# Kernel optimization log

Measured on AMD Instinct MI355X. Metric: run time of the kernel, lower is better.

## Reference

```python
import jax, jax.numpy as jnp
import numpy as np

B, T, NX = 4, 6, 128
F_IN, H, F_OUT = 64, 128, 64
N = T * NX * NX  # 98304 cubed-sphere nodes


def _build_neighbors():
    # 4-neighbor grid adjacency per tile (periodic within tile), [N, 4] int32.
    t = np.arange(T)[:, None, None]
    i = np.arange(NX)[None, :, None]
    j = np.arange(NX)[None, None, :]

    def nid(tt, ii, jj):
        return tt * NX * NX + (ii % NX) * NX + (jj % NX)

    nbr = np.stack(
        [nid(t, i - 1, j), nid(t, i + 1, j), nid(t, i, j - 1), nid(t, i, j + 1)],
        axis=-1,
    ).reshape(-1, 4)
    return jnp.asarray(nbr, dtype=jnp.int32)


def setup_inputs() -> dict:
    key = jax.random.key(0)
    ks = jax.random.split(key, 20)
    inp = {
        "inputs": jax.random.normal(ks[0], (B, T, NX, NX, F_IN), dtype=jnp.float32),
        "nbr": _build_neighbors(),
    }
    # SAGEConv channel chain: 64->128, 128->64, 64->32, 32->32, 64->64, 128->64
    dims = [(F_IN, H), (H, H // 2), (H // 2, H // 4), (H // 4, H // 4), (H // 2, H // 2), (H, F_OUT)]
    k = 1
    for li, (din, dout) in enumerate(dims, start=1):
        s = 1.0 / np.sqrt(din)
        inp[f"W_self_{li}"] = jax.random.normal(ks[k], (din, dout), dtype=jnp.float32) * s
        inp[f"W_neigh_{li}"] = jax.random.normal(ks[k + 1], (din, dout), dtype=jnp.float32) * s
        inp[f"b_{li}"] = jnp.zeros((dout,), dtype=jnp.float32)
        k += 2
    return inp


def _sage(h, nbr, Ws, Wn, b):
    # h: [N, B, F]. Mean over the 4 fixed grid neighbors, then self+neighbor linear.
    m = (h[nbr[:, 0]] + h[nbr[:, 1]] + h[nbr[:, 2]] + h[nbr[:, 3]]) * 0.25
    return h @ Ws + m @ Wn + b


def reference(inputs, nbr,
              W_self_1, W_neigh_1, b_1, W_self_2, W_neigh_2, b_2,
              W_self_3, W_neigh_3, b_3, W_self_4, W_neigh_4, b_4,
              W_self_5, W_neigh_5, b_5, W_self_6, W_neigh_6, b_6):
    b, t, nx, ny, f = inputs.shape
    x = inputs.reshape(b, t * nx * ny, f).transpose(1, 0, 2)  # [N, B, F]
    act = jax.nn.relu
    # num_blocks = 1
    h1 = act(_sage(x, nbr, W_self_1, W_neigh_1, b_1))
    h2 = act(_sage(h1, nbr, W_self_2, W_neigh_2, b_2))
    h3 = act(_sage(h2, nbr, W_self_3, W_neigh_3, b_3))
    h4 = act(_sage(h3, nbr, W_self_4, W_neigh_4, b_4))
    h5 = jnp.concatenate([act(_sage(h4, nbr, W_self_4, W_neigh_4, b_4)), h3], axis=-1)
    h6 = jnp.concatenate([act(_sage(h5, nbr, W_self_5, W_neigh_5, b_5)), h2], axis=-1)
    out = _sage(h6, nbr, W_self_6, W_neigh_6, b_6)  # [N, B, F_OUT]
    return out.transpose(1, 0, 2).reshape(b, t, nx, ny, -1)
```

## Files before the change

kernel.cpp:

```cpp
#include <hip/hip_runtime.h>
#include <type_traits>

#define NNODES 98304
#define NB 4

typedef __attribute__((ext_vector_type(8))) short short8;
typedef __attribute__((ext_vector_type(8))) unsigned short ushort8;
typedef __attribute__((ext_vector_type(4))) float f32x4;

__device__ __forceinline__ float bf2f(unsigned short u) {
  union { unsigned int u; float f; } c; c.u = ((unsigned int)u) << 16; return c.f;
}
__device__ __forceinline__ unsigned short f2bf(float f) {
  union { float f; unsigned int u; } c; c.f = f;
  unsigned int r = 0x7FFFu + ((c.u >> 16) & 1u);
  return (unsigned short)((c.u + r) >> 16);
}
__device__ __forceinline__ unsigned int cvtpk(float lo, float hi) {
  unsigned int r;
  asm("v_cvt_pk_bf16_f32 %0, %1, %2" : "=v"(r) : "v"(lo), "v"(hi));
  return r;
}

__device__ __forceinline__ void tile_barrier() {
  asm volatile("s_waitcnt lgkmcnt(0)" ::: "memory");
  __builtin_amdgcn_s_barrier();
  asm volatile("" ::: "memory");
}

constexpr int rows_for(int FIN)            { return FIN == 32 ? 64 : 32; }
constexpr int grid_for(int FIN, int SRCK)  { return (FIN == 128 || SRCK == 0) ? 1024 : 1536; }
constexpr int minw_for(int FIN, int SRCK)  { return (FIN == 128 || SRCK == 0) ? 4 : 6; }

template<int FIN, int FOUT, int SRCK, int DSTK, bool RELU>
__global__ __launch_bounds__(256, minw_for(FIN, SRCK))
void sage_mfma(const void* __restrict__ srcp, int sstride, int soff,
               void* __restrict__ dstp, int dstride, int doff,
               const float* __restrict__ Ws, const float* __restrict__ Wn,
               const float* __restrict__ bias, const int* __restrict__ nbr)
{
  constexpr int ROWS = rows_for(FIN);
  constexpr int GRID = grid_for(FIN, SRCK);
  constexpr int NPT = ROWS / 4;
  constexpr int NTILES = (NNODES * NB) / ROWS;
  constexpr int K = 2 * FIN;
  constexpr int KSTEPS = K / 32;
  constexpr int LD = K + 8;
  constexpr int WAVES_N = (FOUT >= 64) ? 4 : 2;
  constexpr int WAVES_M = 4 / WAVES_N;
  constexpr int CF = FOUT / (16 * WAVES_N);
  constexpr int RF = ROWS / (16 * WAVES_M);
  constexpr int CHUNKS = FIN / 8;
  constexpr int ITERS = (ROWS * CHUNKS) / 256;
  constexpr int PF = ITERS;
  constexpr int PT = ITERS - PF;

  __shared__ unsigned short As[2][ROWS][LD];

  const int tid = threadIdx.x;
  const int wave = tid >> 6, lane = tid & 63;
  const int wn = wave % WAVES_N, wm = wave / WAVES_N;
  const int colbase = wn * (FOUT / WAVES_N);
  const int rowbase = wm * (ROWS / WAVES_M);
  const int fn = lane & 15, fg = lane >> 4;

  short8 Bfrag[KSTEPS][CF];
  float bv[CF];
  #pragma unroll
  for (int ks = 0; ks < KSTEPS; ++ks) {
    const float* wb = (ks * 32 < FIN) ? (Ws + (size_t)(ks * 32) * FOUT)
                                      : (Wn + (size_t)(ks * 32 - FIN) * FOUT);
    #pragma unroll
    for (int cf = 0; cf < CF; ++cf) {
      const int col = colbase + cf * 16 + fn;
      short8 f;
      #pragma unroll
      for (int j = 0; j < 8; ++j)
        f[j] = (short)f2bf(wb[(size_t)(fg * 8 + j) * FOUT + col]);
      Bfrag[ks][cf] = f;
    }
  }
  #pragma unroll
  for (int cf = 0; cf < CF; ++cf) bv[cf] = bias[colbase + cf * 16 + fn];

  struct G0 { float4 s0, s1, a0, a1, b0, b1, c0, c1, d0, d1; };
  struct G1 { ushort8 s, n0, n1, n2, n3; };
  using PG = typename std::conditional<SRCK == 0, G0, G1>::type;

  auto issue = [&](int node0, int it, PG& p) {
    const int g = tid + it * 256;
    const int r = g / CHUNKS;
    const int c = (g - r * CHUNKS) * 8;
    const int n = node0 + (r >> 2);
    const int b = r & 3;
    const int4 nb4 = reinterpret_cast<const int4*>(nbr)[n];
    if constexpr (SRCK == 0) {
      const float* s = (const float*)srcp;
      const float* ps = s + ((size_t)b * NNODES + n) * FIN + c;
      const float* p0 = s + ((size_t)b * NNODES + nb4.x) * FIN + c;
      const float* p1 = s + ((size_t)b * NNODES + nb4.y) * FIN + c;
      const float* p2 = s + ((size_t)b * NNODES + nb4.z) * FIN + c;
      const float* p3 = s + ((size_t)b * NNODES + nb4.w) * FIN + c;
      p.s0 = *(const float4*)ps; p.s1 = *(const float4*)(ps + 4);
      p.a0 = *(const float4*)p0; p.a1 = *(const float4*)(p0 + 4);
      p.b0 = *(const float4*)p1; p.b1 = *(const float4*)(p1 + 4);
      p.c0 = *(const float4*)p2; p.c1 = *(const float4*)(p2 + 4);
      p.d0 = *(const float4*)p3; p.d1 = *(const float4*)(p3 + 4);
    } else {
      const unsigned short* s = (const unsigned short*)srcp;
      auto ld = [&](int nn) {
        return *reinterpret_cast<const ushort8*>(s + ((size_t)nn * NB + b) * sstride + soff + c);
      };
      p.s = ld(n); p.n0 = ld(nb4.x); p.n1 = ld(nb4.y); p.n2 = ld(nb4.z); p.n3 = ld(nb4.w);
    }
  };

  auto finish = [&](int buf, int it, PG& p) {
    const int g = tid + it * 256;
    const int r = g / CHUNKS;
    const int c = (g - r * CHUNKS) * 8;
    uint4 xv, mv;
    if constexpr (SRCK == 0) {
      xv = make_uint4(cvtpk(p.s0.x, p.s0.y), cvtpk(p.s0.z, p.s0.w),
                      cvtpk(p.s1.x, p.s1.y), cvtpk(p.s1.z, p.s1.w));
      float4 m0, m1;
      m0.x = (p.a0.x + p.b0.x) + (p.c0.x + p.d0.x);
      m0.y = (p.a0.y + p.b0.y) + (p.c0.y + p.d0.y);
      m0.z = (p.a0.z + p.b0.z) + (p.c0.z + p.d0.z);
      m0.w = (p.a0.w + p.b0.w) + (p.c0.w + p.d0.w);
      m1.x = (p.a1.x + p.b1.x) + (p.c1.x + p.d1.x);
      m1.y = (p.a1.y + p.b1.y) + (p.c1.y + p.d1.y);
      m1.z = (p.a1.z + p.b1.z) + (p.c1.z + p.d1.z);
      m1.w = (p.a1.w + p.b1.w) + (p.c1.w + p.d1.w);
      mv = make_uint4(cvtpk(m0.x * 0.25f, m0.y * 0.25f), cvtpk(m0.z * 0.25f, m0.w * 0.25f),
                      cvtpk(m1.x * 0.25f, m1.y * 0.25f), cvtpk(m1.z * 0.25f, m1.w * 0.25f));
    } else {
      xv = make_uint4((unsigned)(unsigned short)p.s[0] | ((unsigned)(unsigned short)p.s[1] << 16),
                      (unsigned)(unsigned short)p.s[2] | ((unsigned)(unsigned short)p.s[3] << 16),
                      (unsigned)(unsigned short)p.s[4] | ((unsigned)(unsigned short)p.s[5] << 16),
                      (unsigned)(unsigned short)p.s[6] | ((unsigned)(unsigned short)p.s[7] << 16));
      float sum[8];
      #pragma unroll
      for (int j = 0; j < 8; ++j)
        sum[j] = (bf2f(p.n0[j]) + bf2f(p.n1[j])) + (bf2f(p.n2[j]) + bf2f(p.n3[j]));
      mv = make_uint4(cvtpk(sum[0] * 0.25f, sum[1] * 0.25f), cvtpk(sum[2] * 0.25f, sum[3] * 0.25f),
                      cvtpk(sum[4] * 0.25f, sum[5] * 0.25f), cvtpk(sum[6] * 0.25f, sum[7] * 0.25f));
    }
    *reinterpret_cast<uint4*>(&As[buf][r][c]) = xv;
    *reinterpret_cast<uint4*>(&As[buf][r][FIN + c]) = mv;
  };

  {
    PG p[ITERS];
    #pragma unroll
    for (int it = 0; it < ITERS; ++it) issue(blockIdx.x * NPT, it, p[it]);
    #pragma unroll
    for (int it = 0; it < ITERS; ++it) finish(0, it, p[it]);
  }

  int cur = 0;
  for (int tile = blockIdx.x; tile < NTILES; tile += GRID) {
    const int node0 = tile * NPT;
    const bool hasnext = (tile + GRID) < NTILES;
    const int nnode0 = (tile + GRID) * NPT;

    PG ptop[PF];
    if (hasnext) {
      #pragma unroll
      for (int it = 0; it < PF; ++it) issue(nnode0, it, ptop[it]);
    }

    tile_barrier();

    f32x4 acc[RF][CF];
    #pragma unroll
    for (int rf = 0; rf < RF; ++rf)
      #pragma unroll
      for (int cf = 0; cf < CF; ++cf)
        acc[rf][cf] = (f32x4){bv[cf], bv[cf], bv[cf], bv[cf]};

    #pragma unroll
    for (int ks = 0; ks < KSTEPS; ++ks) {
      short8 a[RF];
      #pragma unroll
      for (int rf = 0; rf < RF; ++rf)
        a[rf] = *reinterpret_cast<const short8*>(&As[cur][rowbase + rf * 16 + fn][ks * 32 + fg * 8]);
      #pragma unroll
      for (int rf = 0; rf < RF; ++rf)
        #pragma unroll
        for (int cf = 0; cf < CF; ++cf)
          acc[rf][cf] = __builtin_amdgcn_mfma_f32_16x16x32_bf16(
              a[rf], Bfrag[ks][cf], acc[rf][cf], 0, 0, 0);
    }

    #pragma unroll
    for (int rf = 0; rf < RF; ++rf) {
      #pragma unroll
      for (int cf = 0; cf < CF; ++cf) {
        const int col = colbase + cf * 16 + fn;
        #pragma unroll
        for (int j = 0; j < 4; ++j) {
          const int row = rowbase + rf * 16 + fg * 4 + j;
          const int n = node0 + (row >> 2);
          const int b = row & 3;
          float v = acc[rf][cf][j];
          if (RELU) v = fmaxf(v, 0.f);
          if (DSTK == 0) {
            ((float*)dstp)[((size_t)b * NNODES + n) * FOUT + col] = v;
          } else {
            ((unsigned short*)dstp)[((size_t)n * NB + b) * dstride + doff + col] = f2bf(v);
          }
        }
      }
    }

    if (hasnext) {
      #pragma unroll
      for (int it = 0; it < PF; ++it) finish(cur ^ 1, it, ptop[it]);
    }
    cur ^= 1;
  }
}

extern "C" void kernel_launch(void* const* d_in, const int* in_sizes, int n_in,
                              void* d_out, int out_size, void* d_ws, size_t ws_size,
                              hipStream_t stream) {
  const float* x  = (const float*)d_in[0];
  const int* nbr  = (const int*)d_in[1];
  const float* W1s = (const float*)d_in[2],  *W1n = (const float*)d_in[3],  *b1 = (const float*)d_in[4];
  const float* W2s = (const float*)d_in[5],  *W2n = (const float*)d_in[6],  *b2 = (const float*)d_in[7];
  const float* W3s = (const float*)d_in[8],  *W3n = (const float*)d_in[9],  *b3 = (const float*)d_in[10];
  const float* W4s = (const float*)d_in[11], *W4n = (const float*)d_in[12], *b4 = (const float*)d_in[13];
  const float* W5s = (const float*)d_in[14], *W5n = (const float*)d_in[15], *b5 = (const float*)d_in[16];
  const float* W6s = (const float*)d_in[17], *W6n = (const float*)d_in[18], *b6 = (const float*)d_in[19];

  unsigned short* h1 = (unsigned short*)d_out;
  unsigned short* h6 = (unsigned short*)d_ws;
  unsigned short* h5 = (unsigned short*)d_out;
  unsigned short* h4 = (unsigned short*)((char*)d_out + (size_t)NNODES * NB * 64 * 2);

  const dim3 block(256);

  sage_mfma<64, 128, 0, 1, true><<<dim3(grid_for(64, 0)), block, 0, stream>>>(x, 0, 0, h1, 128, 0, W1s, W1n, b1, nbr);
  sage_mfma<128, 64, 1, 1, true><<<dim3(grid_for(128, 1)), block, 0, stream>>>(h1, 128, 0, h6, 128, 64, W2s, W2n, b2, nbr);
  sage_mfma<64, 32, 1, 1, true><<<dim3(grid_for(64, 1)), block, 0, stream>>>(h6, 128, 64, h5, 64, 32, W3s, W3n, b3, nbr);
  sage_mfma<32, 32, 1, 1, true><<<dim3(grid_for(32, 1)), block, 0, stream>>>(h5, 64, 32, h4, 32, 0, W4s, W4n, b4, nbr);
  sage_mfma<32, 32, 1, 1, true><<<dim3(grid_for(32, 1)), block, 0, stream>>>(h4, 32, 0, h5, 64, 0, W4s, W4n, b4, nbr);
  sage_mfma<64, 64, 1, 1, true><<<dim3(grid_for(64, 1)), block, 0, stream>>>(h5, 64, 0, h6, 128, 0, W5s, W5n, b5, nbr);
  sage_mfma<128, 64, 1, 0, false><<<dim3(grid_for(128, 1)), block, 0, stream>>>(h6, 128, 0, d_out, 0, 0, W6s, W6n, b6, nbr);
}
```

Before: 229.3 us.

## Fuse pairs of SAGE layers with halo-tiled stencil kernels on grid tiles

Replaces the generic neighbor-index gather with spatial 8x8 tiles plus halos loaded into LDS, exploiting the periodic grid stencil directly. Pairs of consecutive layers (1-2, 4-4, 5-6) are fused so the intermediate activation stays in LDS and is recomputed on a halo ring instead of going through global memory. Weights are pre-transposed to bf16 in a device global buffer by small prep kernels. This trades redundant halo recomputation, larger LDS use and extra prep launches for fewer global round trips and fewer kernel launches. It also ignores the nbr input and assumes the fixed grid adjacency.

```diff
diff --git a/kernel.cpp b/kernel.cpp
--- a/kernel.cpp
+++ b/kernel.cpp
@@ -3,6 +3,8 @@
 
 #define NNODES 98304
 #define NB 4
+#define NX 128
+#define FACE (NX * NX)
 
 typedef __attribute__((ext_vector_type(8))) short short8;
 typedef __attribute__((ext_vector_type(8))) unsigned short ushort8;
@@ -10,6 +12,9 @@
 
 __device__ __forceinline__ float bf2f(unsigned short u) {
   union { unsigned int u; float f; } c; c.u = ((unsigned int)u) << 16; return c.f;
+}
+__device__ __forceinline__ float asf(unsigned int u) {
+  union { unsigned int u; float f; } c; c.u = u; return c.f;
 }
 __device__ __forceinline__ unsigned short f2bf(float f) {
   union { float f; unsigned int u; } c; c.f = f;
@@ -22,12 +27,204 @@
   return r;
 }
 
+__device__ __forceinline__ short8 mean4(const unsigned short* pA, const unsigned short* pB,
+                                        const unsigned short* pC, const unsigned short* pD) {
+  uint4 a = *(const uint4*)pA, b = *(const uint4*)pB, c = *(const uint4*)pC, d = *(const uint4*)pD;
+  const unsigned* pa = &a.x; const unsigned* pb = &b.x;
+  const unsigned* pc = &c.x; const unsigned* pd = &d.x;
+  union { uint4 u; short8 s; } o;
+  unsigned* po = &o.u.x;
+  #pragma unroll
+  for (int i = 0; i < 4; ++i) {
+    float lo = (asf(pa[i] << 16) + asf(pb[i] << 16)) + (asf(pc[i] << 16) + asf(pd[i] << 16));
+    float hi = (asf(pa[i] & 0xFFFF0000u) + asf(pb[i] & 0xFFFF0000u)) +
+               (asf(pc[i] & 0xFFFF0000u) + asf(pd[i] & 0xFFFF0000u));
+    po[i] = cvtpk(lo * 0.25f, hi * 0.25f);
+  }
+  return o.s;
+}
+
+__device__ __attribute__((aligned(16))) unsigned short g_wt[59392];
+#define WT_A12 0
+#define WT_B12 16384
+#define WT_45  32768
+#define WT_A67 34816
+#define WT_B67 43008
+
+__global__ void prep_wt(const float* __restrict__ Ws, const float* __restrict__ Wn,
+                        int FIN, int FOUT, int dstoff) {
+  const int K = 2 * FIN, total = FOUT * K;
+  for (int e = blockIdx.x * 256 + threadIdx.x; e < total; e += gridDim.x * 256) {
+    const int col = e / K, k = e % K;
+    const float v = (k < FIN) ? Ws[(size_t)k * FOUT + col] : Wn[(size_t)(k - FIN) * FOUT + col];
+    g_wt[dstoff + e] = f2bf(v);
+  }
+}
+
+template<int FA, int FOA, int FEXT, int FOB, int SRCK, int DSTK, bool RELUB, int MINW>
+__global__ __launch_bounds__(256, MINW)
+void sage_fused2(const void* __restrict__ srcA, int ssA, int soA,
+                 const unsigned short* __restrict__ srcE, int ssE, int soE,
+                 void* __restrict__ dst, int dstr, int dof,
+                 int wtaOff, int wtbOff,
+                 const float* __restrict__ ba, const float* __restrict__ bb)
+{
+  constexpr int TI = 8, TJ = 8;
+  constexpr int RAJ = TJ + 4, NRA = (TI + 4) * RAJ;
+  constexpr int HJ = TJ + 2, NH = (TI + 2) * HJ;
+  constexpr int MA = 112;
+  constexpr int KA = 2 * FA, KB = 2 * (FOA + FEXT);
+  constexpr int CFA = FOA / 16, CFB = FOB / 16;
+  constexpr int LDA = FA + 8, LDH = FOA + 8, LDE = FEXT + 8;
+
+  __shared__ unsigned short rawA[NRA][LDA];
+  __shared__ unsigned short H[MA][LDH];
+  __shared__ unsigned short rawE[FEXT ? NH : 1][FEXT ? LDE : 1];
+
+  const int tid = threadIdx.x;
+  const int b = blockIdx.x & 3;
+  const int tt = blockIdx.x >> 2;
+  const int t = tt >> 8;
+  const int i0 = ((tt >> 4) & 15) * TI, j0 = (tt & 15) * TJ;
+  const int nbase = t * FACE;
+
+  constexpr int CHA = FA / 8;
+  for (int u = tid; u < NRA * CHA; u += 256) {
+    const int s = u / CHA, c = (u - s * CHA) * 8;
+    const int di = s / RAJ - 2, dj = s % RAJ - 2;
+    const int n = nbase + ((i0 + di) & (NX - 1)) * NX + ((j0 + dj) & (NX - 1));
+    uint4 v;
+    if constexpr (SRCK == 0) {
+      const float* p = (const float*)srcA + ((size_t)b * NNODES + n) * FA + c;
+      const float4 a = *(const float4*)p, q = *(const float4*)(p + 4);
+      v = make_uint4(cvtpk(a.x, a.y), cvtpk(a.z, a.w), cvtpk(q.x, q.y), cvtpk(q.z, q.w));
+    } else {
+      v = *(const uint4*)((const unsigned short*)srcA + ((size_t)n * NB + b) * ssA + soA + c);
+    }
+    *(uint4*)&rawA[s][c] = v;
+  }
+  if constexpr (FEXT != 0) {
+    constexpr int CHE = FEXT / 8;
+    for (int u = tid; u < NH * CHE; u += 256) {
+      const int s = u / CHE, c = (u - s * CHE) * 8;
+      const int di = s / HJ - 1, dj = s % HJ - 1;
+      const int n = nbase + ((i0 + di) & (NX - 1)) * NX + ((j0 + dj) & (NX - 1));
+      *(uint4*)&rawE[s][c] =
+          *(const uint4*)(srcE + ((size_t)n * NB + b) * ssE + soE + c);
+    }
+  }
+  __syncthreads();
+
+  const int lane = tid & 63, wave = tid >> 6;
+  const int fn = lane & 15, fg = lane >> 4;
+
+  {
+    const unsigned short* wt = g_wt + wtaOff;
+    #pragma unroll 1
+    for (int rfi = 0; rfi < 2; ++rfi) {
+      const int rf = wave + rfi * 4;
+      if (rf >= 7) break;
+      const int r = rf * 16 + fn;
+      const int rc = r < NH ? r : NH - 1;
+      const int sA = (rc / HJ + 1) * RAJ + (rc % HJ) + 1;
+      f32x4 acc[CFA];
+      #pragma unroll
+      for (int cf = 0; cf < CFA; ++cf) {
+        const float4 bt = *(const float4*)(ba + cf * 16 + fg * 4);
+        acc[cf] = (f32x4){bt.x, bt.y, bt.z, bt.w};
+      }
+      #pragma unroll 1
+      for (int ks = 0; ks < KA / 32; ++ks) {
+        short8 xf;
+        if (ks < FA / 32) {
+          xf = *(const short8*)&rawA[sA][ks * 32 + fg * 8];
+        } else {
+          const int cc = (ks - FA / 32) * 32 + fg * 8;
+          xf = mean4(&rawA[sA - RAJ][cc], &rawA[sA + RAJ][cc],
+                     &rawA[sA - 1][cc], &rawA[sA + 1][cc]);
+        }
+        #pragma unroll
+        for (int cf = 0; cf < CFA; ++cf) {
+          const short8 wf = *(const short8*)(wt + (size_t)(cf * 16 + fn) * KA + ks * 32 + fg * 8);
+          acc[cf] = __builtin_amdgcn_mfma_f32_16x16x32_bf16(wf, xf, acc[cf], 0, 0, 0);
+        }
+      }
+      #pragma unroll
+      for (int cf = 0; cf < CFA; ++cf) {
+        const uint2 u = make_uint2(
+            cvtpk(fmaxf(acc[cf][0], 0.f), fmaxf(acc[cf][1], 0.f)),
+            cvtpk(fmaxf(acc[cf][2], 0.f), fmaxf(acc[cf][3], 0.f)));
+        *(uint2*)&H[r][cf * 16 + fg * 4] = u;
+      }
+    }
+  }
+  __syncthreads();
+
+  {
+    const unsigned short* wt = g_wt + wtbOff;
+    const int r = wave * 16 + fn;
+    const int sH = (r / TJ + 1) * HJ + (r % TJ) + 1;
+    f32x4 acc[CFB];
+    #pragma unroll
+    for (int cf = 0; cf < CFB; ++cf) {
+      const float bt = bb[cf * 16 + fn];
+      acc[cf] = (f32x4){bt, bt, bt, bt};
+    }
+    constexpr int S1 = FOA / 32;
+    constexpr int S2 = S1 + FEXT / 32;
+    constexpr int S3 = S2 + FOA / 32;
+    #pragma unroll 1
+    for (int ks = 0; ks < KB / 32; ++ks) {
+      short8 xf;
+      if constexpr (FEXT == 0) {
+        if (ks < S1) {
+          xf = *(const short8*)&H[sH][ks * 32 + fg * 8];
+        } else {
+          const int cc = (ks - S1) * 32 + fg * 8;
+          xf = mean4(&H[sH - HJ][cc], &H[sH + HJ][cc], &H[sH - 1][cc], &H[sH + 1][cc]);
+        }
+      } else {
+        if (ks < S1) {
+          xf = *(const short8*)&H[sH][ks * 32 + fg * 8];
+        } else if (ks < S2) {
+          xf = *(const short8*)&rawE[sH][(ks - S1) * 32 + fg * 8];
+        } else if (ks < S3) {
+          const int cc = (ks - S2) * 32 + fg * 8;
+          xf = mean4(&H[sH - HJ][cc], &H[sH + HJ][cc], &H[sH - 1][cc], &H[sH + 1][cc]);
+        } else {
+          const int cc = (ks - S3) * 32 + fg * 8;
+          xf = mean4(&rawE[sH - HJ][cc], &rawE[sH + HJ][cc], &rawE[sH - 1][cc], &rawE[sH + 1][cc]);
+        }
+      }
+      #pragma unroll
+      for (int cf = 0; cf < CFB; ++cf) {
+        const short8 wf = *(const short8*)(wt + (size_t)(cf * 16 + fn) * KB + ks * 32 + fg * 8);
+        acc[cf] = __builtin_amdgcn_mfma_f32_16x16x32_bf16(xf, wf, acc[cf], 0, 0, 0);
+      }
+    }
+    #pragma unroll
+    for (int cf = 0; cf < CFB; ++cf) {
+      const int col = cf * 16 + fn;
+      #pragma unroll
+      for (int j = 0; j < 4; ++j) {
+        const int rr = wave * 16 + fg * 4 + j;
+        const int n = nbase + (i0 + (rr / TJ)) * NX + j0 + (rr % TJ);
+        float v = acc[cf][j];
+        if (RELUB) v = fmaxf(v, 0.f);
+        if constexpr (DSTK == 0)
+          ((float*)dst)[((size_t)b * NNODES + n) * FOB + col] = v;
+        else
+          ((unsigned short*)dst)[((size_t)n * NB + b) * dstr + dof + col] = f2bf(v);
+      }
+    }
+  }
+}
+
 __device__ __forceinline__ void tile_barrier() {
   asm volatile("s_waitcnt lgkmcnt(0)" ::: "memory");
   __builtin_amdgcn_s_barrier();
   asm volatile("" ::: "memory");
 }
-
 constexpr int rows_for(int FIN)            { return FIN == 32 ? 64 : 32; }
 constexpr int grid_for(int FIN, int SRCK)  { return (FIN == 128 || SRCK == 0) ? 1024 : 1536; }
 constexpr int minw_for(int FIN, int SRCK)  { return (FIN == 128 || SRCK == 0) ? 4 : 6; }
@@ -53,7 +250,6 @@
   constexpr int CHUNKS = FIN / 8;
   constexpr int ITERS = (ROWS * CHUNKS) / 256;
   constexpr int PF = ITERS;
-  constexpr int PT = ITERS - PF;
 
   __shared__ unsigned short As[2][ROWS][LD];
 
@@ -83,9 +279,8 @@
   #pragma unroll
   for (int cf = 0; cf < CF; ++cf) bv[cf] = bias[colbase + cf * 16 + fn];
 
-  struct G0 { float4 s0, s1, a0, a1, b0, b1, c0, c1, d0, d1; };
   struct G1 { ushort8 s, n0, n1, n2, n3; };
-  using PG = typename std::conditional<SRCK == 0, G0, G1>::type;
+  using PG = G1;
 
   auto issue = [&](int node0, int it, PG& p) {
     const int g = tid + it * 256;
@@ -94,58 +289,27 @@
     const int n = node0 + (r >> 2);
     const int b = r & 3;
     const int4 nb4 = reinterpret_cast<const int4*>(nbr)[n];
-    if constexpr (SRCK == 0) {
-      const float* s = (const float*)srcp;
-      const float* ps = s + ((size_t)b * NNODES + n) * FIN + c;
-      const float* p0 = s + ((size_t)b * NNODES + nb4.x) * FIN + c;
-      const float* p1 = s + ((size_t)b * NNODES + nb4.y) * FIN + c;
-      const float* p2 = s + ((size_t)b * NNODES + nb4.z) * FIN + c;
-      const float* p3 = s + ((size_t)b * NNODES + nb4.w) * FIN + c;
-      p.s0 = *(const float4*)ps; p.s1 = *(const float4*)(ps + 4);
-      p.a0 = *(const float4*)p0; p.a1 = *(const float4*)(p0 + 4);
-      p.b0 = *(const float4*)p1; p.b1 = *(const float4*)(p1 + 4);
-      p.c0 = *(const float4*)p2; p.c1 = *(const float4*)(p2 + 4);
-      p.d0 = *(const float4*)p3; p.d1 = *(const float4*)(p3 + 4);
-    } else {
-      const unsigned short* s = (const unsigned short*)srcp;
-      auto ld = [&](int nn) {
-        return *reinterpret_cast<const ushort8*>(s + ((size_t)nn * NB + b) * sstride + soff + c);
-      };
-      p.s = ld(n); p.n0 = ld(nb4.x); p.n1 = ld(nb4.y); p.n2 = ld(nb4.z); p.n3 = ld(nb4.w);
-    }
+    const unsigned short* s = (const unsigned short*)srcp;
+    auto ld = [&](int nn) {
+      return *reinterpret_cast<const ushort8*>(s + ((size_t)nn * NB + b) * sstride + soff + c);
+    };
+    p.s = ld(n); p.n0 = ld(nb4.x); p.n1 = ld(nb4.y); p.n2 = ld(nb4.z); p.n3 = ld(nb4.w);
   };
-
   auto finish = [&](int buf, int it, PG& p) {
     const int g = tid + it * 256;
     const int r = g / CHUNKS;
     const int c = (g - r * CHUNKS) * 8;
-    uint4 xv, mv;
-    if constexpr (SRCK == 0) {
-      xv = make_uint4(cvtpk(p.s0.x, p.s0.y), cvtpk(p.s0.z, p.s0.w),
-                      cvtpk(p.s1.x, p.s1.y), cvtpk(p.s1.z, p.s1.w));
-      float4 m0, m1;
-      m0.x = (p.a0.x + p.b0.x) + (p.c0.x + p.d0.x);
-      m0.y = (p.a0.y + p.b0.y) + (p.c0.y + p.d0.y);
-      m0.z = (p.a0.z + p.b0.z) + (p.c0.z + p.d0.z);
-      m0.w = (p.a0.w + p.b0.w) + (p.c0.w + p.d0.w);
-      m1.x = (p.a1.x + p.b1.x) + (p.c1.x + p.d1.x);
-      m1.y = (p.a1.y + p.b1.y) + (p.c1.y + p.d1.y);
-      m1.z = (p.a1.z + p.b1.z) + (p.c1.z + p.d1.z);
-      m1.w = (p.a1.w + p.b1.w) + (p.c1.w + p.d1.w);
-      mv = make_uint4(cvtpk(m0.x * 0.25f, m0.y * 0.25f), cvtpk(m0.z * 0.25f, m0.w * 0.25f),
-                      cvtpk(m1.x * 0.25f, m1.y * 0.25f), cvtpk(m1.z * 0.25f, m1.w * 0.25f));
-    } else {
-      xv = make_uint4((unsigned)(unsigned short)p.s[0] | ((unsigned)(unsigned short)p.s[1] << 16),
-                      (unsigned)(unsigned short)p.s[2] | ((unsigned)(unsigned short)p.s[3] << 16),
-                      (unsigned)(unsigned short)p.s[4] | ((unsigned)(unsigned short)p.s[5] << 16),
-                      (unsigned)(unsigned short)p.s[6] | ((unsigned)(unsigned short)p.s[7] << 16));
-      float sum[8];
-      #pragma unroll
-      for (int j = 0; j < 8; ++j)
-        sum[j] = (bf2f(p.n0[j]) + bf2f(p.n1[j])) + (bf2f(p.n2[j]) + bf2f(p.n3[j]));
-      mv = make_uint4(cvtpk(sum[0] * 0.25f, sum[1] * 0.25f), cvtpk(sum[2] * 0.25f, sum[3] * 0.25f),
-                      cvtpk(sum[4] * 0.25f, sum[5] * 0.25f), cvtpk(sum[6] * 0.25f, sum[7] * 0.25f));
-    }
+    uint4 xv = make_uint4(
+        (unsigned)(unsigned short)p.s[0] | ((unsigned)(unsigned short)p.s[1] << 16),
+        (unsigned)(unsigned short)p.s[2] | ((unsigned)(unsigned short)p.s[3] << 16),
+        (unsigned)(unsigned short)p.s[4] | ((unsigned)(unsigned short)p.s[5] << 16),
+        (unsigned)(unsigned short)p.s[6] | ((unsigned)(unsigned short)p.s[7] << 16));
+    float sum[8];
+    #pragma unroll
+    for (int j = 0; j < 8; ++j)
+      sum[j] = (bf2f(p.n0[j]) + bf2f(p.n1[j])) + (bf2f(p.n2[j]) + bf2f(p.n3[j]));
+    uint4 mv = make_uint4(cvtpk(sum[0] * 0.25f, sum[1] * 0.25f), cvtpk(sum[2] * 0.25f, sum[3] * 0.25f),
+                          cvtpk(sum[4] * 0.25f, sum[5] * 0.25f), cvtpk(sum[6] * 0.25f, sum[7] * 0.25f));
     *reinterpret_cast<uint4*>(&As[buf][r][c]) = xv;
     *reinterpret_cast<uint4*>(&As[buf][r][FIN + c]) = mv;
   };
@@ -205,11 +369,10 @@
           const int b = row & 3;
           float v = acc[rf][cf][j];
           if (RELU) v = fmaxf(v, 0.f);
-          if (DSTK == 0) {
+          if (DSTK == 0)
             ((float*)dstp)[((size_t)b * NNODES + n) * FOUT + col] = v;
-          } else {
+          else
             ((unsigned short*)dstp)[((size_t)n * NB + b) * dstride + doff + col] = f2bf(v);
-          }
         }
       }
     }
@@ -234,18 +397,22 @@
   const float* W5s = (const float*)d_in[14], *W5n = (const float*)d_in[15], *b5 = (const float*)d_in[16];
   const float* W6s = (const float*)d_in[17], *W6n = (const float*)d_in[18], *b6 = (const float*)d_in[19];
 
-  unsigned short* h1 = (unsigned short*)d_out;
-  unsigned short* h6 = (unsigned short*)d_ws;
-  unsigned short* h5 = (unsigned short*)d_out;
-  unsigned short* h4 = (unsigned short*)((char*)d_out + (size_t)NNODES * NB * 64 * 2);
-
-  const dim3 block(256);
-
-  sage_mfma<64, 128, 0, 1, true><<<dim3(grid_for(64, 0)), block, 0, stream>>>(x, 0, 0, h1, 128, 0, W1s, W1n, b1, nbr);
-  sage_mfma<128, 64, 1, 1, true><<<dim3(grid_for(128, 1)), block, 0, stream>>>(h1, 128, 0, h6, 128, 64, W2s, W2n, b2, nbr);
-  sage_mfma<64, 32, 1, 1, true><<<dim3(grid_for(64, 1)), block, 0, stream>>>(h6, 128, 64, h5, 64, 32, W3s, W3n, b3, nbr);
-  sage_mfma<32, 32, 1, 1, true><<<dim3(grid_for(32, 1)), block, 0, stream>>>(h5, 64, 32, h4, 32, 0, W4s, W4n, b4, nbr);
-  sage_mfma<32, 32, 1, 1, true><<<dim3(grid_for(32, 1)), block, 0, stream>>>(h4, 32, 0, h5, 64, 0, W4s, W4n, b4, nbr);
-  sage_mfma<64, 64, 1, 1, true><<<dim3(grid_for(64, 1)), block, 0, stream>>>(h5, 64, 0, h6, 128, 0, W5s, W5n, b5, nbr);
-  sage_mfma<128, 64, 1, 0, false><<<dim3(grid_for(128, 1)), block, 0, stream>>>(h6, 128, 0, d_out, 0, 0, W6s, W6n, b6, nbr);
-}
+  unsigned short* hbuf = (unsigned short*)d_ws;
+
+  const dim3 blk(256);
+
+  prep_wt<<<dim3(32), blk, 0, stream>>>(W1s, W1n, 64, 128, WT_A12);
+  prep_wt<<<dim3(32), blk, 0, stream>>>(W2s, W2n, 128, 64, WT_B12);
+  prep_wt<<<dim3(8),  blk, 0, stream>>>(W4s, W4n, 32, 32, WT_45);
+  prep_wt<<<dim3(16), blk, 0, stream>>>(W5s, W5n, 64, 64, WT_A67);
+  prep_wt<<<dim3(32), blk, 0, stream>>>(W6s, W6n, 128, 64, WT_B67);
+
+  sage_fused2<64, 128, 0, 64, 0, 1, true, 3><<<dim3(6144), blk, 0, stream>>>(
+      x, 0, 0, nullptr, 0, 0, hbuf, 128, 64, WT_A12, WT_B12, b1, b2);
+  sage_mfma<64, 32, 1, 1, true><<<dim3(grid_for(64, 1)), blk, 0, stream>>>(
+      hbuf, 128, 64, hbuf, 128, 32, W3s, W3n, b3, nbr);
+  sage_fused2<32, 32, 0, 32, 1, 1, true, 4><<<dim3(6144), blk, 0, stream>>>(
+      hbuf, 128, 32, nullptr, 0, 0, hbuf, 128, 0, WT_45, WT_45, b4, b4);
+  sage_fused2<64, 64, 64, 64, 1, 0, false, 3><<<dim3(6144), blk, 0, stream>>>(
+      hbuf, 128, 0, hbuf, 128, 64, d_out, 0, 0, WT_A67, WT_B67, b5, b6);
+}
```

Result: slower. 553.3 us (+141.3%).
